# Optimization experiments

Hardware: AMD Instinct MI355X
Metric: run time of the kernel (lower is better)

The kernel has to match this reference:

```python
import jax, jax.numpy as jnp
import numpy as np

B, S, E, H = 2, 2048, 1024, 16
D = E // H  # head_dim = 64


def setup_inputs() -> dict:
    key = jax.random.key(0)
    k1, k2, k3 = jax.random.split(key, 3)
    scale = 0.02  # GPT-2 init scale
    return {
        "hidden_states": jax.random.normal(k1, (B, S, E), dtype=jnp.float32),
        "c_attn_w": jax.random.normal(k2, (E, 3 * E), dtype=jnp.float32) * scale,
        "c_attn_b": jnp.zeros((3 * E,), dtype=jnp.float32),
        "c_proj_w": jax.random.normal(k3, (E, E), dtype=jnp.float32) * scale,
        "c_proj_b": jnp.zeros((E,), dtype=jnp.float32),
    }


def reference(hidden_states, c_attn_w, c_attn_b, c_proj_w, c_proj_b):
    # Conv1D: x @ W + b  -> qkv [B, S, 3E]
    qkv = hidden_states @ c_attn_w + c_attn_b
    q, k, v = jnp.split(qkv, 3, axis=-1)

    # split heads -> [B, H, S, D]
    def split_heads(t):
        return t.reshape(B, S, H, D).transpose(0, 2, 1, 3)

    q, k, v = split_heads(q), split_heads(k), split_heads(v)

    # naive full attention: QK^T / sqrt(D) -> softmax -> @ V
    attn_weights = jnp.einsum("bhqd,bhkd->bhqk", q, k) / jnp.sqrt(
        jnp.asarray(D, dtype=q.dtype)
    )
    attn_weights = jax.nn.softmax(attn_weights, axis=-1)
    attn_output = jnp.einsum("bhqk,bhkd->bhqd", attn_weights, v)

    # merge heads -> [B, S, E], then output projection
    attn_output = attn_output.transpose(0, 2, 1, 3).reshape(B, S, E)
    attn_output = attn_output @ c_proj_w + c_proj_b
    return attn_output
```

## Files before the change

### kernel.cpp

```cpp
#include <hip/hip_runtime.h>

#define SEQ 2048
#define EMB 1024
#define KDIM 1024
#define CF 0.180336880111113f

typedef __attribute__((ext_vector_type(8))) short short8_t;
typedef __attribute__((ext_vector_type(4))) float floatx4;
typedef __attribute__((ext_vector_type(4))) unsigned short ushort4_t;
typedef __attribute__((ext_vector_type(4))) unsigned int uivec4;

#define GLOAD16(gp, lp)                                                        \
  __builtin_amdgcn_global_load_lds(                                            \
      (const __attribute__((address_space(1))) void*)(gp),                     \
      (__attribute__((address_space(3))) void*)(lp), 16, 0, 0)

#define WGBAR()                                   \
  do {                                            \
    __asm__ __volatile__("" ::: "memory");        \
    __builtin_amdgcn_s_barrier();                 \
    __asm__ __volatile__("" ::: "memory");        \
  } while (0)

static __device__ __forceinline__ unsigned short f2bf(float x) {
  unsigned int u = __float_as_uint(x);
  return (unsigned short)((u + 0x7fffu + ((u >> 16) & 1u)) >> 16);
}

static __device__ __forceinline__ short8_t mk_pb(unsigned int a, unsigned int b,
                                                 unsigned int c, unsigned int d) {
  uivec4 t;
  t[0] = a; t[1] = b; t[2] = c; t[3] = d;
  return __builtin_bit_cast(short8_t, t);
}

static __device__ __forceinline__ unsigned int pack_bf(float p0, float p1) {
  return __builtin_amdgcn_perm(__float_as_uint(p1), __float_as_uint(p0),
                               0x07060302u);
}

static __device__ __forceinline__ void tconv_tile(
    const float* __restrict__ W, unsigned short* __restrict__ T, int N, int K,
    int n0, int k0, int tid) {
  __shared__ float Tl[64][65];
  const int lx = tid & 15, ly = tid >> 4;
#pragma unroll
  for (int u = 0; u < 4; ++u) {
    int r = u * 16 + ly;
    float4 v = *(const float4*)&W[(size_t)(k0 + r) * N + n0 + lx * 4];
    Tl[r][lx * 4 + 0] = v.x;
    Tl[r][lx * 4 + 1] = v.y;
    Tl[r][lx * 4 + 2] = v.z;
    Tl[r][lx * 4 + 3] = v.w;
  }
  __syncthreads();
#pragma unroll
  for (int u = 0; u < 4; ++u) {
    int n = u * 16 + ly;
    ushort4_t h;
#pragma unroll
    for (int v = 0; v < 4; ++v) h[v] = f2bf(Tl[lx * 4 + v][n]);
    *(ushort4_t*)&T[(size_t)(n0 + n) * K + k0 + lx * 4] = h;
  }
}

__global__ __launch_bounds__(256) void prep(
    const float* __restrict__ hs, const float* __restrict__ caw,
    const float* __restrict__ cpw, unsigned short* __restrict__ hsb,
    unsigned short* __restrict__ w1t, unsigned short* __restrict__ w2t) {
  const int bid = blockIdx.x, tid = threadIdx.x;
  if (bid < 4096) {
    const int i = bid * 256 + tid;
    float4 v = *(const float4*)&hs[(size_t)i * 4];
    ushort4_t h = {f2bf(v.x), f2bf(v.y), f2bf(v.z), f2bf(v.w)};
    *(ushort4_t*)&hsb[(size_t)i * 4] = h;
  } else if (bid < 4864) {
    const int idx = bid - 4096;
    tconv_tile(caw, w1t, 3 * EMB, EMB, (idx % 48) * 64, (idx / 48) * 64, tid);
  } else {
    const int idx = bid - 4864;
    tconv_tile(cpw, w2t, EMB, EMB, (idx % 16) * 64, (idx / 16) * 64, tid);
  }
}

template <int MODE, int BN>
__global__ __launch_bounds__(256) void gemm_pl(
    const unsigned short* __restrict__ Ag, const unsigned short* __restrict__ Bg,
    const float* __restrict__ bias, float* __restrict__ outF,
    unsigned short* __restrict__ qk, unsigned short* __restrict__ vt) {
  __shared__ __attribute__((aligned(16))) unsigned short Ah[3][128 * 32];
  __shared__ __attribute__((aligned(16))) unsigned short Bh[3][BN * 32];
  const int NJ = BN / 32;

  const int tid = threadIdx.x;
  const int w = tid >> 6, lane = tid & 63;
  const int quad = lane >> 4, c = lane & 15;

  int bm, bn;
  {
    const int L = blockIdx.x, x = L & 7, g = L >> 3;
    if (MODE == 0) {
      bm = ((x & 1) * 16 + (g & 15)) * 128;
      bn = ((x >> 1) * 6 + (g >> 4)) * 128;
    } else {
      bm = ((x & 3) * 8 + (g & 7)) * 128;
      bn = ((x >> 2) * 8 + (g >> 3)) * 64;
    }
  }
  const int wm = (w >> 1) * 64, wn = (w & 1) * (BN / 2);

  const unsigned short* gsrc = (w < 2) ? Ag : Bg;
  const int lbo = (w < 2) ? (w & 1) * 64 * 32 : (w & 1) * (BN / 2) * 32;
  const int rbase = (w < 2) ? (bm + (w & 1) * 64) : (bn + (w & 1) * (BN / 2));
  const int nloads = (w < 2) ? 4 : (BN / 32);
  const int srow = lane >> 2;
  const int sblk = (lane & 3) ^ ((lane >> 3) & 3);
  const char* gp0 = (const char*)(gsrc + (size_t)(rbase + srow) * KDIM) + sblk * 16;

  floatx4 acc[4][NJ];
  const floatx4 z = {0.f, 0.f, 0.f, 0.f};
#pragma unroll
  for (int i = 0; i < 4; ++i)
#pragma unroll
    for (int j = 0; j < NJ; ++j) acc[i][j] = z;

  const int sw = (c >> 1) & 3;

#define STAGE_G(buf, kt)                                                       \
  do {                                                                         \
    unsigned short* ld = ((w < 2) ? Ah[buf] : Bh[buf]) + lbo;                  \
    const char* gp = gp0 + (size_t)(kt) * 64;                                  \
    for (int i_ = 0; i_ < nloads; ++i_)                                        \
      GLOAD16(gp + (size_t)i_ * 16 * (KDIM * 2), &ld[i_ * 512]);               \
  } while (0)

  STAGE_G(0, 0);
  STAGE_G(1, 1);

  for (int t = 0; t < 32; ++t) {
    if (BN == 128 || w < 2) {
      __asm__ __volatile__("s_waitcnt vmcnt(4)" ::: "memory");
    } else {
      __asm__ __volatile__("s_waitcnt vmcnt(2)" ::: "memory");
    }
    WGBAR();
    STAGE_G((t + 2) % 3, (t + 2) & 31);
    const unsigned short* Ac = Ah[t % 3];
    const unsigned short* Bc = Bh[t % 3];

    const int oct = (quad ^ sw) * 8;
    short8_t a[4], b[NJ];
#pragma unroll
    for (int i = 0; i < 4; ++i)
      a[i] = *(const short8_t*)&Ac[(wm + 16 * i + c) * 32 + oct];
#pragma unroll
    for (int j = 0; j < NJ; ++j)
      b[j] = *(const short8_t*)&Bc[(wn + 16 * j + c) * 32 + oct];
#pragma unroll
    for (int i = 0; i < 4; ++i)
#pragma unroll
      for (int j = 0; j < NJ; ++j)
        acc[i][j] = __builtin_amdgcn_mfma_f32_16x16x32_bf16(b[j], a[i], acc[i][j], 0, 0, 0);
  }
#undef STAGE_G

  __asm__ __volatile__("s_waitcnt vmcnt(0)" ::: "memory");

#pragma unroll
  for (int i = 0; i < 4; ++i) {
    const int row = bm + wm + 16 * i + c;
#pragma unroll
    for (int j = 0; j < NJ; ++j) {
      const int col0 = bn + wn + 16 * j + quad * 4;
      floatx4 v = acc[i][j] + *(const floatx4*)&bias[col0];
      if (MODE == 0) {
        if (col0 < 1024) v = v * CF;
        if (col0 < 2048) {
          ushort4_t pk = {f2bf(v[0]), f2bf(v[1]), f2bf(v[2]), f2bf(v[3])};
          *(ushort4_t*)&qk[(size_t)row * 2048 + col0] = pk;
        } else {
          const int c2 = col0 - 2048, hh = c2 >> 6, d0 = c2 & 63;
          const int bb = row >> 11, s = row & 2047;
          const int j = s & 63;
          const int lam = (j & 0x20) | ((j & 0x0C) << 1) | ((j & 0x10) >> 2) | (j & 3);
          const int sp = (s & ~63) | lam;
          unsigned short* vb = &vt[((size_t)(bb * 16 + hh) * 64 + d0) * 2048 + sp];
          vb[0 * 2048] = f2bf(v[0]);
          vb[1 * 2048] = f2bf(v[1]);
          vb[2 * 2048] = f2bf(v[2]);
          vb[3 * 2048] = f2bf(v[3]);
        }
      } else {
        *(floatx4*)&outF[(size_t)row * 1024 + col0] = v;
      }
    }
  }
}

static __device__ __forceinline__ void stage_kv(
    int w, int srow, int sblkg, const unsigned short* __restrict__ gK,
    const unsigned short* __restrict__ gV, unsigned short* Kbuf,
    unsigned short* Vbuf, int jt) {
  if (w < 2) {
    const unsigned short* g0 = gK + (size_t)(jt * 64 + w * 32 + srow) * 2048 + sblkg * 8;
    unsigned short* l0 = &Kbuf[(w * 32) * 64];
#pragma unroll
    for (int i = 0; i < 4; ++i) GLOAD16(g0 + (size_t)i * 8 * 2048, &l0[i * 512]);
  } else {
    const unsigned short* g0 = gV + (size_t)((w - 2) * 32 + srow) * 2048 + jt * 64 + sblkg * 8;
    unsigned short* l0 = &Vbuf[((w - 2) * 32) * 64];
#pragma unroll
    for (int i = 0; i < 4; ++i) GLOAD16(g0 + (size_t)i * 8 * 2048, &l0[i * 512]);
  }
}

__global__ __launch_bounds__(256) void attn7(
    const unsigned short* __restrict__ qk, const unsigned short* __restrict__ vt,
    unsigned short* __restrict__ ao) {
  __shared__ __attribute__((aligned(16))) unsigned short SMEM[6 * 4096];
  unsigned short* Ksb = SMEM;
  unsigned short* Vsb = SMEM + 3 * 4096;

  const int tid = threadIdx.x;
  const int w = tid >> 6, lane = tid & 63, quad = lane >> 4, c = lane & 15;
  const int qh = w >> 1, kh = w & 1;
  const int q0 = blockIdx.x * 128, h = blockIdx.y, b = blockIdx.z;
  const int rk = c & 7;

  short8_t qf[4][2];
  {
    const size_t rb = (size_t)b * SEQ + q0 + qh * 64;
#pragma unroll
    for (int mi = 0; mi < 4; ++mi) {
      const size_t qr = (rb + mi * 16 + c) * 2048 + h * 64 + quad * 8;
      qf[mi][0] = *(const short8_t*)&qk[qr];
      qf[mi][1] = *(const short8_t*)&qk[qr + 32];
    }
  }
  __asm__ __volatile__("s_waitcnt vmcnt(0)" ::: "memory");

  floatx4 O[4][4], Osum[4];
  const floatx4 z = {0.f, 0.f, 0.f, 0.f};
#pragma unroll
  for (int mi = 0; mi < 4; ++mi) {
    Osum[mi] = z;
#pragma unroll
    for (int dg = 0; dg < 4; ++dg) O[mi][dg] = z;
  }
  short8_t ones;
#pragma unroll
  for (int e = 0; e < 8; ++e) ones[e] = (short)0x3F80;

  const int srow = lane >> 3;
  const int sblkg = (lane & 7) ^ srow;
  const unsigned short* gK = qk + (size_t)b * SEQ * 2048 + 1024 + h * 64;
  const unsigned short* gV = vt + (size_t)(b * 16 + h) * 64 * 2048;

  stage_kv(w, srow, sblkg, gK, gV, Ksb, Vsb, 0);
  stage_kv(w, srow, sblkg, gK, gV, Ksb + 4096, Vsb + 4096, 1);

  for (int t = 0; t < 32; ++t) {
    __asm__ __volatile__("s_waitcnt vmcnt(4)" ::: "memory");
    WGBAR();
    stage_kv(w, srow, sblkg, gK, gV, Ksb + ((t + 2) % 3) * 4096,
             Vsb + ((t + 2) % 3) * 4096, (t + 2) & 31);
    const unsigned short* Kc = Ksb + (t % 3) * 4096;
    const unsigned short* Vc = Vsb + (t % 3) * 4096;

    floatx4 S[4][2];
#pragma unroll
    for (int mi = 0; mi < 4; ++mi)
#pragma unroll
      for (int jg = 0; jg < 2; ++jg) S[mi][jg] = z;
#pragma unroll
    for (int kd = 0; kd < 2; ++kd) {
      const int oct = ((4 * kd + quad) ^ rk) * 8;
#pragma unroll
      for (int jg = 0; jg < 2; ++jg) {
        short8_t kf = *(const short8_t*)&Kc[((kh * 2 + jg) * 16 + c) * 64 + oct];
#pragma unroll
        for (int mi = 0; mi < 4; ++mi)
          S[mi][jg] = __builtin_amdgcn_mfma_f32_16x16x32_bf16(kf, qf[mi][kd], S[mi][jg], 0, 0, 0);
      }
    }

    unsigned int pw[4][2][2];
#pragma unroll
    for (int mi = 0; mi < 4; ++mi)
#pragma unroll
      for (int jg = 0; jg < 2; ++jg) {
        float p0 = __builtin_amdgcn_exp2f(S[mi][jg][0]);
        float p1 = __builtin_amdgcn_exp2f(S[mi][jg][1]);
        float p2 = __builtin_amdgcn_exp2f(S[mi][jg][2]);
        float p3 = __builtin_amdgcn_exp2f(S[mi][jg][3]);
        pw[mi][jg][0] = pack_bf(p0, p1);
        pw[mi][jg][1] = pack_bf(p2, p3);
      }

    const int octv = ((4 * kh + quad) ^ rk) * 8;
    short8_t pb[4];
#pragma unroll
    for (int mi = 0; mi < 4; ++mi) {
      pb[mi] = mk_pb(pw[mi][0][0], pw[mi][0][1], pw[mi][1][0], pw[mi][1][1]);
      Osum[mi] = __builtin_amdgcn_mfma_f32_16x16x32_bf16(ones, pb[mi], Osum[mi], 0, 0, 0);
    }
#pragma unroll
    for (int dg = 0; dg < 4; ++dg) {
      short8_t vf = *(const short8_t*)&Vc[(dg * 16 + c) * 64 + octv];
#pragma unroll
      for (int mi = 0; mi < 4; ++mi)
        O[mi][dg] = __builtin_amdgcn_mfma_f32_16x16x32_bf16(vf, pb[mi], O[mi][dg], 0, 0, 0);
    }
  }

  __asm__ __volatile__("s_waitcnt vmcnt(0)" ::: "memory");
  WGBAR();

  float* Of = (float*)SMEM;
  float* Ss = (float*)(SMEM + 17408);
  if (kh == 1) {
#pragma unroll
    for (int mi = 0; mi < 4; ++mi) {
      const int row = mi * 16 + c;
      float* orow = &Of[(qh * 64 + row) * 68];
#pragma unroll
      for (int dg = 0; dg < 4; ++dg)
        *(floatx4*)&orow[dg * 16 + quad * 4] = O[mi][dg];
      if (quad == 0) Ss[qh * 64 + row] = Osum[mi][0];
    }
  }
  WGBAR();
  if (kh == 0) {
#pragma unroll
    for (int mi = 0; mi < 4; ++mi) {
      const int row = mi * 16 + c;
      const float inv = 1.0f / (Osum[mi][0] + Ss[qh * 64 + row]);
      const float* orow = &Of[(qh * 64 + row) * 68];
      const size_t grow = (size_t)b * SEQ + q0 + qh * 64 + row;
#pragma unroll
      for (int dg = 0; dg < 4; ++dg) {
        floatx4 o = O[mi][dg] + *(const floatx4*)&orow[dg * 16 + quad * 4];
        ushort4_t ov = {f2bf(o[0] * inv), f2bf(o[1] * inv),
                        f2bf(o[2] * inv), f2bf(o[3] * inv)};
        *(ushort4_t*)&ao[grow * EMB + h * 64 + dg * 16 + quad * 4] = ov;
      }
    }
  }
}

extern "C" void kernel_launch(void* const* d_in, const int* in_sizes, int n_in,
                              void* d_out, int out_size, void* d_ws, size_t ws_size,
                              hipStream_t stream) {
  const float* hs = (const float*)d_in[0];
  const float* c_attn_w = (const float*)d_in[1];
  const float* c_attn_b = (const float*)d_in[2];
  const float* c_proj_w = (const float*)d_in[3];
  const float* c_proj_b = (const float*)d_in[4];
  float* out = (float*)d_out;

  char* ws = (char*)d_ws;
  unsigned short* hsb = (unsigned short*)(ws + 0);
  unsigned short* qk  = (unsigned short*)(ws + 8388608);
  unsigned short* vt  = (unsigned short*)(ws + 25165824);
  unsigned short* aob = (unsigned short*)(ws + 33554432);
  unsigned short* w1t = (unsigned short*)(ws + 41943040);
  unsigned short* w2t = (unsigned short*)(ws + 48234496);

  prep<<<5120, 256, 0, stream>>>(hs, c_attn_w, c_proj_w, hsb, w1t, w2t);
  gemm_pl<0, 128><<<768, 256, 0, stream>>>(hsb, w1t, c_attn_b, nullptr, qk, vt);
  attn7<<<dim3(16, 16, 2), 256, 0, stream>>>(qk, vt, aob);
  gemm_pl<2, 64><<<512, 256, 0, stream>>>(aob, w2t, c_proj_b, out, nullptr, nullptr);
}
```

Before: 176.1 us.

## Enlarge attention blocks to 256 queries and switch GEMM to double buffering

The attention kernel now runs 512-thread blocks covering 256 query rows. K/V staging is shared by eight waves, blocks are remapped so a group of blocks shares a head, and the P·V loop is fused per row tile to shorten register live ranges. The GEMMs drop from a three-stage to a two-stage LDS pipeline that waits for all loads each iteration, with a launch-bounds occupancy hint. This cuts K/V reloads and LDS use but exposes more global-load latency in the GEMMs and halves the attention grid.

```diff
diff --git a/kernel.cpp b/kernel.cpp
--- a/kernel.cpp
+++ b/kernel.cpp
@@ -84,12 +84,12 @@
 }
 
 template <int MODE, int BN>
-__global__ __launch_bounds__(256) void gemm_pl(
+__global__ __launch_bounds__(256, 4) void gemm_pl(
     const unsigned short* __restrict__ Ag, const unsigned short* __restrict__ Bg,
     const float* __restrict__ bias, float* __restrict__ outF,
     unsigned short* __restrict__ qk, unsigned short* __restrict__ vt) {
-  __shared__ __attribute__((aligned(16))) unsigned short Ah[3][128 * 32];
-  __shared__ __attribute__((aligned(16))) unsigned short Bh[3][BN * 32];
+  __shared__ __attribute__((aligned(16))) unsigned short Ah[2][128 * 32];
+  __shared__ __attribute__((aligned(16))) unsigned short Bh[2][BN * 32];
   const int NJ = BN / 32;
 
   const int tid = threadIdx.x;
@@ -135,18 +135,13 @@
   } while (0)
 
   STAGE_G(0, 0);
-  STAGE_G(1, 1);
 
   for (int t = 0; t < 32; ++t) {
-    if (BN == 128 || w < 2) {
-      __asm__ __volatile__("s_waitcnt vmcnt(4)" ::: "memory");
-    } else {
-      __asm__ __volatile__("s_waitcnt vmcnt(2)" ::: "memory");
-    }
+    __asm__ __volatile__("s_waitcnt vmcnt(0)" ::: "memory");
     WGBAR();
-    STAGE_G((t + 2) % 3, (t + 2) & 31);
-    const unsigned short* Ac = Ah[t % 3];
-    const unsigned short* Bc = Bh[t % 3];
+    if (t < 31) STAGE_G((t + 1) & 1, t + 1);
+    const unsigned short* Ac = Ah[t & 1];
+    const unsigned short* Bc = Bh[t & 1];
 
     const int oct = (quad ^ sw) * 8;
     short8_t a[4], b[NJ];
@@ -163,8 +158,6 @@
         acc[i][j] = __builtin_amdgcn_mfma_f32_16x16x32_bf16(b[j], a[i], acc[i][j], 0, 0, 0);
   }
 #undef STAGE_G
-
-  __asm__ __volatile__("s_waitcnt vmcnt(0)" ::: "memory");
 
 #pragma unroll
   for (int i = 0; i < 4; ++i) {
@@ -197,34 +190,39 @@
   }
 }
 
-static __device__ __forceinline__ void stage_kv(
+static __device__ __forceinline__ void stage_kv16(
     int w, int srow, int sblkg, const unsigned short* __restrict__ gK,
     const unsigned short* __restrict__ gV, unsigned short* Kbuf,
     unsigned short* Vbuf, int jt) {
-  if (w < 2) {
-    const unsigned short* g0 = gK + (size_t)(jt * 64 + w * 32 + srow) * 2048 + sblkg * 8;
-    unsigned short* l0 = &Kbuf[(w * 32) * 64];
-#pragma unroll
-    for (int i = 0; i < 4; ++i) GLOAD16(g0 + (size_t)i * 8 * 2048, &l0[i * 512]);
+  if (w < 4) {
+    const unsigned short* g0 =
+        gK + (size_t)(jt * 64 + w * 16 + srow) * 2048 + sblkg * 8;
+    unsigned short* l0 = &Kbuf[(w * 16) * 64];
+    GLOAD16(g0, l0);
+    GLOAD16(g0 + (size_t)8 * 2048, l0 + 8 * 64);
   } else {
-    const unsigned short* g0 = gV + (size_t)((w - 2) * 32 + srow) * 2048 + jt * 64 + sblkg * 8;
-    unsigned short* l0 = &Vbuf[((w - 2) * 32) * 64];
-#pragma unroll
-    for (int i = 0; i < 4; ++i) GLOAD16(g0 + (size_t)i * 8 * 2048, &l0[i * 512]);
-  }
-}
-
-__global__ __launch_bounds__(256) void attn7(
+    const unsigned short* g0 =
+        gV + (size_t)((w - 4) * 16 + srow) * 2048 + jt * 64 + sblkg * 8;
+    unsigned short* l0 = &Vbuf[((w - 4) * 16) * 64];
+    GLOAD16(g0, l0);
+    GLOAD16(g0 + (size_t)8 * 2048, l0 + 8 * 64);
+  }
+}
+
+__global__ __launch_bounds__(512, 1) void attn10(
     const unsigned short* __restrict__ qk, const unsigned short* __restrict__ vt,
     unsigned short* __restrict__ ao) {
-  __shared__ __attribute__((aligned(16))) unsigned short SMEM[6 * 4096];
-  unsigned short* Ksb = SMEM;
-  unsigned short* Vsb = SMEM + 3 * 4096;
+  __shared__ __attribute__((aligned(16))) unsigned short KV[6 * 4096];
+  unsigned short* Ksb = KV;
+  unsigned short* Vsb = KV + 3 * 4096;
 
   const int tid = threadIdx.x;
   const int w = tid >> 6, lane = tid & 63, quad = lane >> 4, c = lane & 15;
   const int qh = w >> 1, kh = w & 1;
-  const int q0 = blockIdx.x * 128, h = blockIdx.y, b = blockIdx.z;
+  const int L = blockIdx.x, x = L & 7, g = L >> 3;
+  const int hb = x * 4 + (g >> 3);
+  const int h = hb & 15, b = hb >> 4;
+  const int q0 = (g & 7) * 256;
   const int rk = c & 7;
 
   short8_t qf[4][2];
@@ -256,14 +254,16 @@
   const unsigned short* gK = qk + (size_t)b * SEQ * 2048 + 1024 + h * 64;
   const unsigned short* gV = vt + (size_t)(b * 16 + h) * 64 * 2048;
 
-  stage_kv(w, srow, sblkg, gK, gV, Ksb, Vsb, 0);
-  stage_kv(w, srow, sblkg, gK, gV, Ksb + 4096, Vsb + 4096, 1);
+  stage_kv16(w, srow, sblkg, gK, gV, Ksb, Vsb, 0);
+  stage_kv16(w, srow, sblkg, gK, gV, Ksb + 4096, Vsb + 4096, 1);
+
+  const int octv = ((4 * kh + quad) ^ rk) * 8;
 
   for (int t = 0; t < 32; ++t) {
-    __asm__ __volatile__("s_waitcnt vmcnt(4)" ::: "memory");
+    __asm__ __volatile__("s_waitcnt vmcnt(2)" ::: "memory");
     WGBAR();
-    stage_kv(w, srow, sblkg, gK, gV, Ksb + ((t + 2) % 3) * 4096,
-             Vsb + ((t + 2) % 3) * 4096, (t + 2) & 31);
+    stage_kv16(w, srow, sblkg, gK, gV, Ksb + ((t + 2) % 3) * 4096,
+               Vsb + ((t + 2) % 3) * 4096, (t + 2) & 31);
     const unsigned short* Kc = Ksb + (t % 3) * 4096;
     const unsigned short* Vc = Vsb + (t % 3) * 4096;
 
@@ -284,67 +284,64 @@
       }
     }
 
-    unsigned int pw[4][2][2];
-#pragma unroll
-    for (int mi = 0; mi < 4; ++mi)
+#pragma unroll
+    for (int mi = 0; mi < 4; ++mi) {
+      unsigned int pw[2][2];
 #pragma unroll
       for (int jg = 0; jg < 2; ++jg) {
         float p0 = __builtin_amdgcn_exp2f(S[mi][jg][0]);
         float p1 = __builtin_amdgcn_exp2f(S[mi][jg][1]);
         float p2 = __builtin_amdgcn_exp2f(S[mi][jg][2]);
         float p3 = __builtin_amdgcn_exp2f(S[mi][jg][3]);
-        pw[mi][jg][0] = pack_bf(p0, p1);
-        pw[mi][jg][1] = pack_bf(p2, p3);
-      }
-
-    const int octv = ((4 * kh + quad) ^ rk) * 8;
-    short8_t pb[4];
-#pragma unroll
-    for (int mi = 0; mi < 4; ++mi) {
-      pb[mi] = mk_pb(pw[mi][0][0], pw[mi][0][1], pw[mi][1][0], pw[mi][1][1]);
-      Osum[mi] = __builtin_amdgcn_mfma_f32_16x16x32_bf16(ones, pb[mi], Osum[mi], 0, 0, 0);
-    }
-#pragma unroll
-    for (int dg = 0; dg < 4; ++dg) {
-      short8_t vf = *(const short8_t*)&Vc[(dg * 16 + c) * 64 + octv];
-#pragma unroll
-      for (int mi = 0; mi < 4; ++mi)
-        O[mi][dg] = __builtin_amdgcn_mfma_f32_16x16x32_bf16(vf, pb[mi], O[mi][dg], 0, 0, 0);
+        pw[jg][0] = pack_bf(p0, p1);
+        pw[jg][1] = pack_bf(p2, p3);
+      }
+      short8_t pb = mk_pb(pw[0][0], pw[0][1], pw[1][0], pw[1][1]);
+      Osum[mi] = __builtin_amdgcn_mfma_f32_16x16x32_bf16(ones, pb, Osum[mi], 0, 0, 0);
+#pragma unroll
+      for (int dg = 0; dg < 4; ++dg) {
+        short8_t vf = *(const short8_t*)&Vc[(dg * 16 + c) * 64 + octv];
+        O[mi][dg] = __builtin_amdgcn_mfma_f32_16x16x32_bf16(vf, pb, O[mi][dg], 0, 0, 0);
+      }
     }
   }
 
   __asm__ __volatile__("s_waitcnt vmcnt(0)" ::: "memory");
   WGBAR();
 
-  float* Of = (float*)SMEM;
-  float* Ss = (float*)(SMEM + 17408);
-  if (kh == 1) {
-#pragma unroll
-    for (int mi = 0; mi < 4; ++mi) {
-      const int row = mi * 16 + c;
-      float* orow = &Of[(qh * 64 + row) * 68];
-#pragma unroll
-      for (int dg = 0; dg < 4; ++dg)
-        *(floatx4*)&orow[dg * 16 + quad * 4] = O[mi][dg];
-      if (quad == 0) Ss[qh * 64 + row] = Osum[mi][0];
-    }
-  }
-  WGBAR();
-  if (kh == 0) {
-#pragma unroll
-    for (int mi = 0; mi < 4; ++mi) {
-      const int row = mi * 16 + c;
-      const float inv = 1.0f / (Osum[mi][0] + Ss[qh * 64 + row]);
-      const float* orow = &Of[(qh * 64 + row) * 68];
-      const size_t grow = (size_t)b * SEQ + q0 + qh * 64 + row;
-#pragma unroll
-      for (int dg = 0; dg < 4; ++dg) {
-        floatx4 o = O[mi][dg] + *(const floatx4*)&orow[dg * 16 + quad * 4];
-        ushort4_t ov = {f2bf(o[0] * inv), f2bf(o[1] * inv),
-                        f2bf(o[2] * inv), f2bf(o[3] * inv)};
-        *(ushort4_t*)&ao[grow * EMB + h * 64 + dg * 16 + quad * 4] = ov;
-      }
-    }
+  float* Of = (float*)KV;
+  float* Ss2 = (float*)((char*)KV + 34816);
+#pragma unroll
+  for (int p = 0; p < 2; ++p) {
+    if (kh == 1 && (qh >> 1) == p) {
+#pragma unroll
+      for (int mi = 0; mi < 4; ++mi) {
+        const int row = (qh & 1) * 64 + mi * 16 + c;
+        float* orow = &Of[row * 68];
+#pragma unroll
+        for (int dg = 0; dg < 4; ++dg)
+          *(floatx4*)&orow[dg * 16 + quad * 4] = O[mi][dg];
+        if (quad == 0) Ss2[row] = Osum[mi][0];
+      }
+    }
+    WGBAR();
+    if (kh == 0 && (qh >> 1) == p) {
+#pragma unroll
+      for (int mi = 0; mi < 4; ++mi) {
+        const int row = (qh & 1) * 64 + mi * 16 + c;
+        const float inv = 1.0f / (Osum[mi][0] + Ss2[row]);
+        const float* orow = &Of[row * 68];
+        const size_t grow = (size_t)b * SEQ + q0 + qh * 64 + mi * 16 + c;
+#pragma unroll
+        for (int dg = 0; dg < 4; ++dg) {
+          floatx4 o = O[mi][dg] + *(const floatx4*)&orow[dg * 16 + quad * 4];
+          ushort4_t ov = {f2bf(o[0] * inv), f2bf(o[1] * inv),
+                          f2bf(o[2] * inv), f2bf(o[3] * inv)};
+          *(ushort4_t*)&ao[grow * EMB + h * 64 + dg * 16 + quad * 4] = ov;
+        }
+      }
+    }
+    WGBAR();
   }
 }
 
@@ -368,6 +365,6 @@
 
   prep<<<5120, 256, 0, stream>>>(hs, c_attn_w, c_proj_w, hsb, w1t, w2t);
   gemm_pl<0, 128><<<768, 256, 0, stream>>>(hsb, w1t, c_attn_b, nullptr, qk, vt);
-  attn7<<<dim3(16, 16, 2), 256, 0, stream>>>(qk, vt, aob);
+  attn10<<<256, 512, 0, stream>>>(qk, vt, aob);
   gemm_pl<2, 64><<<512, 256, 0, stream>>>(aob, w2t, c_proj_b, out, nullptr, nullptr);
 }
```

Result: no change. 175.8 us (-0.2%).
